# Optimization experiments

Measured on AMD Instinct MI355X. Metric: run time of the kernel, lower is better.

## Reference

```python
import jax, jax.numpy as jnp
import numpy as np

N = 100000      # number of nodes
D = 64          # node_dim
H = 128         # hidden
E = 1600000     # number of undirected edges (each yields 2 directed messages)


def setup_inputs() -> dict:
    key = jax.random.key(0)
    k_nodes, k_edges, k_w1, k_w2 = jax.random.split(key, 4)
    nodes = jax.random.normal(k_nodes, (N, D), dtype=jnp.float32)
    edges = jax.random.randint(k_edges, (E, 2), 0, N, dtype=jnp.int32)
    # msg = Linear(2D, H) -> ReLU -> Linear(H, D); Kaiming-ish init
    W1 = jax.random.normal(k_w1, (2 * D, H), dtype=jnp.float32) * (1.0 / np.sqrt(2 * D))
    b1 = jnp.zeros((H,), dtype=jnp.float32)
    W2 = jax.random.normal(k_w2, (H, D), dtype=jnp.float32) * (1.0 / np.sqrt(H))
    b2 = jnp.zeros((D,), dtype=jnp.float32)
    return {"nodes": nodes, "edges": edges, "W1": W1, "b1": b1, "W2": W2, "b2": b2}


def reference(nodes, edges, W1, b1, W2, b2):
    # nodes: [N, D]; edges: [E, 2] int32
    i = edges[:, 0]
    j = edges[:, 1]
    h_i = nodes[i]            # [E, D] gather
    h_j = nodes[j]            # [E, D] gather

    def mlp(x):               # [E, 2D] -> [E, D]
        return jax.nn.relu(x @ W1 + b1) @ W2 + b2

    m_ij = mlp(jnp.concatenate([h_i, h_j], axis=-1))  # message to node i
    m_ji = mlp(jnp.concatenate([h_j, h_i], axis=-1))  # message to node j

    # out = nodes.clone(); out[i] += m_ij; out[j] += m_ji  (all from ORIGINAL nodes)
    out = nodes \
        + jax.ops.segment_sum(m_ij, i, num_segments=N) \
        + jax.ops.segment_sum(m_ji, j, num_segments=N)
    return out
```

## Files before the change

kernel.cpp:

```cpp
#include <hip/hip_runtime.h>

#define DFEAT 64
#define NEDGES 1600000

typedef __bf16 bf16x8 __attribute__((ext_vector_type(8)));
typedef float f32x4 __attribute__((ext_vector_type(4)));

__device__ __forceinline__ __bf16 f2bf(float f) {
  unsigned u = __builtin_bit_cast(unsigned, f);
  u += 0x7FFFu + ((u >> 16) & 1u);
  unsigned short s = (unsigned short)(u >> 16);
  return __builtin_bit_cast(__bf16, s);
}

__global__ void init_out(const float* __restrict__ nodes, float* __restrict__ out) {
  int i = blockIdx.x * blockDim.x + threadIdx.x;
  ((float4*)out)[i] = ((const float4*)nodes)[i];
}

__launch_bounds__(256, 2)
__global__ void edge_mlp(const float* __restrict__ nodes,
                         const int* __restrict__ edges,
                         const float* __restrict__ W1,
                         const float* __restrict__ b1,
                         const float* __restrict__ W2,
                         const float* __restrict__ b2,
                         float* __restrict__ out) {
  __shared__ __bf16 w1t[128 * 128];
  __shared__ __bf16 w2t[64 * 128];
  __shared__ __bf16 hid[4][16 * 128];

  const int tid = threadIdx.x;

  for (int it = 0; it < 16; ++it) {
    int q = it * 256 + tid;
    int k = q >> 5;
    int nc = (q & 31) << 2;
    float4 v = ((const float4*)W1)[q];
    float vv[4] = {v.x, v.y, v.z, v.w};
#pragma unroll
    for (int c = 0; c < 4; ++c) {
      int n = nc + c;
      int blk = (k >> 3) ^ (n & 15);
      w1t[n * 128 + blk * 8 + (k & 7)] = f2bf(vv[c]);
    }
  }
  for (int it = 0; it < 8; ++it) {
    int q = it * 256 + tid;
    int k = q >> 4;
    int nc = (q & 15) << 2;
    float4 v = ((const float4*)W2)[q];
    float vv[4] = {v.x, v.y, v.z, v.w};
#pragma unroll
    for (int c = 0; c < 4; ++c) {
      int n = nc + c;
      int blk = (k >> 3) ^ (n & 15);
      w2t[n * 128 + blk * 8 + (k & 7)] = f2bf(vv[c]);
    }
  }
  __syncthreads();

  const int lane = tid & 63;
  const int wave = tid >> 6;
  const int col = lane & 15;
  const int quad = lane >> 4;
  __bf16* myhid = hid[wave];

  float b1v[8], b2v[4];
#pragma unroll
  for (int nt = 0; nt < 8; ++nt) b1v[nt] = b1[nt * 16 + col];
#pragma unroll
  for (int nt = 0; nt < 4; ++nt) b2v[nt] = b2[nt * 16 + col];

  for (int t = 0; t < 8; ++t) {
    const int e0 = blockIdx.x * 512 + wave * 128 + t * 16;
    const int e = e0 + col;
    const int ie = edges[2 * e];
    const int je = edges[2 * e + 1];

    bf16x8 af[4];
#pragma unroll
    for (int kt = 0; kt < 4; ++kt) {
      int k = kt * 32 + quad * 8;
      const float* src = (k < 64) ? (nodes + (long)ie * 64 + k)
                                  : (nodes + (long)je * 64 + (k - 64));
      float4 v0 = ((const float4*)src)[0];
      float4 v1 = ((const float4*)src)[1];
      bf16x8 a;
      a[0] = f2bf(v0.x); a[1] = f2bf(v0.y); a[2] = f2bf(v0.z); a[3] = f2bf(v0.w);
      a[4] = f2bf(v1.x); a[5] = f2bf(v1.y); a[6] = f2bf(v1.z); a[7] = f2bf(v1.w);
      af[kt] = a;
    }

#pragma unroll
    for (int dir = 0; dir < 2; ++dir) {
      f32x4 acc[8];
#pragma unroll
      for (int nt = 0; nt < 8; ++nt) acc[nt] = (f32x4)0.0f;
#pragma unroll
      for (int kt = 0; kt < 4; ++kt) {
        int kblk = kt * 4 + quad;
        if (dir) kblk ^= 8;
#pragma unroll
        for (int nt = 0; nt < 8; ++nt) {
          int n = nt * 16 + col;
          const bf16x8 bf = *(const bf16x8*)&w1t[n * 128 + ((kblk ^ (n & 15)) << 3)];
          acc[nt] = __builtin_amdgcn_mfma_f32_16x16x32_bf16(af[kt], bf, acc[nt], 0, 0, 0);
        }
      }
#pragma unroll
      for (int nt = 0; nt < 8; ++nt) {
        int unit = nt * 16 + col;
#pragma unroll
        for (int r = 0; r < 4; ++r) {
          int m = quad * 4 + r;
          float h = acc[nt][r] + b1v[nt];
          h = h > 0.0f ? h : 0.0f;
          myhid[m * 128 + (((unit >> 3) ^ m) << 3) + (unit & 7)] = f2bf(h);
        }
      }

      f32x4 acc2[4];
#pragma unroll
      for (int nt = 0; nt < 4; ++nt) acc2[nt] = (f32x4)0.0f;
#pragma unroll
      for (int kt = 0; kt < 4; ++kt) {
        int kblk = kt * 4 + quad;
        const bf16x8 ah = *(const bf16x8*)&myhid[col * 128 + ((kblk ^ col) << 3)];
#pragma unroll
        for (int nt = 0; nt < 4; ++nt) {
          int n = nt * 16 + col;
          const bf16x8 bf = *(const bf16x8*)&w2t[n * 128 + ((kblk ^ (n & 15)) << 3)];
          acc2[nt] = __builtin_amdgcn_mfma_f32_16x16x32_bf16(ah, bf, acc2[nt], 0, 0, 0);
        }
      }

#pragma unroll
      for (int r = 0; r < 4; ++r) {
        int em = quad * 4 + r;
        int node = __shfl(dir == 0 ? ie : je, em, 64);
        float* dst = out + (long)node * 64;
#pragma unroll
        for (int nt = 0; nt < 4; ++nt) {
          atomicAdd(dst + nt * 16 + col, acc2[nt][r] + b2v[nt]);
        }
      }
    }
  }
}

extern "C" void kernel_launch(void* const* d_in, const int* in_sizes, int n_in,
                              void* d_out, int out_size, void* d_ws, size_t ws_size,
                              hipStream_t stream) {
  const float* nodes = (const float*)d_in[0];
  const int*   edges = (const int*)d_in[1];
  const float* W1    = (const float*)d_in[2];
  const float* b1    = (const float*)d_in[3];
  const float* W2    = (const float*)d_in[4];
  const float* b2    = (const float*)d_in[5];
  float* out = (float*)d_out;

  init_out<<<6250, 256, 0, stream>>>(nodes, out);
  edge_mlp<<<3125, 256, 0, stream>>>(nodes, edges, W1, b1, W2, b2, out);
}
```

Measured before the change: 773.6 us.

## Compute both edge directions together with transposed MFMA and 512-thread blocks

Swaps the first-layer MFMA operands so the weights become the A operand and the gathered features the B operand, with bias preloaded into the accumulators. Both message directions are computed in one pass, so each W1 and W2 fragment loaded from LDS feeds two MFMAs, and hidden activations are written as packed bf16x4 stores. Blocks grow to 512 threads with eight waves sharing one copy of the weights in LDS, which cuts per-block weight staging. Edge indices are loaded as int2. The cost is higher register pressure from keeping two sets of accumulators live, and the launch bounds now ask for 4 blocks of 512 threads per CU.

Result: slower. 2.231 ms (+188.4%).

```diff
diff --git a/kernel.cpp b/kernel.cpp
--- a/kernel.cpp
+++ b/kernel.cpp
@@ -1,9 +1,7 @@
 #include <hip/hip_runtime.h>
 
-#define DFEAT 64
-#define NEDGES 1600000
-
 typedef __bf16 bf16x8 __attribute__((ext_vector_type(8)));
+typedef __bf16 bf16x4 __attribute__((ext_vector_type(4)));
 typedef float f32x4 __attribute__((ext_vector_type(4)));
 
 __device__ __forceinline__ __bf16 f2bf(float f) {
@@ -18,7 +16,7 @@
   ((float4*)out)[i] = ((const float4*)nodes)[i];
 }
 
-__launch_bounds__(256, 2)
+__launch_bounds__(512, 4)
 __global__ void edge_mlp(const float* __restrict__ nodes,
                          const int* __restrict__ edges,
                          const float* __restrict__ W1,
@@ -26,36 +24,36 @@
                          const float* __restrict__ W2,
                          const float* __restrict__ b2,
                          float* __restrict__ out) {
-  __shared__ __bf16 w1t[128 * 128];
+  __shared__ __bf16 w1a[128 * 128];
   __shared__ __bf16 w2t[64 * 128];
-  __shared__ __bf16 hid[4][16 * 128];
+  __shared__ __bf16 hid[8][16 * 128];
 
   const int tid = threadIdx.x;
 
-  for (int it = 0; it < 16; ++it) {
-    int q = it * 256 + tid;
+#pragma unroll
+  for (int it = 0; it < 8; ++it) {
+    int q = it * 512 + tid;
     int k = q >> 5;
-    int nc = (q & 31) << 2;
+    int u0 = (q & 31) << 2;
     float4 v = ((const float4*)W1)[q];
     float vv[4] = {v.x, v.y, v.z, v.w};
 #pragma unroll
     for (int c = 0; c < 4; ++c) {
-      int n = nc + c;
-      int blk = (k >> 3) ^ (n & 15);
-      w1t[n * 128 + blk * 8 + (k & 7)] = f2bf(vv[c]);
+      int u = u0 + c;
+      w1a[u * 128 + (((k >> 3) ^ (u & 15)) << 3) + (k & 7)] = f2bf(vv[c]);
     }
   }
-  for (int it = 0; it < 8; ++it) {
-    int q = it * 256 + tid;
+#pragma unroll
+  for (int it = 0; it < 4; ++it) {
+    int q = it * 512 + tid;
     int k = q >> 4;
-    int nc = (q & 15) << 2;
+    int n0 = (q & 15) << 2;
     float4 v = ((const float4*)W2)[q];
     float vv[4] = {v.x, v.y, v.z, v.w};
 #pragma unroll
     for (int c = 0; c < 4; ++c) {
-      int n = nc + c;
-      int blk = (k >> 3) ^ (n & 15);
-      w2t[n * 128 + blk * 8 + (k & 7)] = f2bf(vv[c]);
+      int n = n0 + c;
+      w2t[n * 128 + (((k >> 3) ^ (n & 15)) << 3) + (k & 7)] = f2bf(vv[c]);
     }
   }
   __syncthreads();
@@ -65,85 +63,104 @@
   const int col = lane & 15;
   const int quad = lane >> 4;
   __bf16* myhid = hid[wave];
+  const float4* b1q = (const float4*)b1;
 
-  float b1v[8], b2v[4];
-#pragma unroll
-  for (int nt = 0; nt < 8; ++nt) b1v[nt] = b1[nt * 16 + col];
+  float b2v[4];
 #pragma unroll
   for (int nt = 0; nt < 4; ++nt) b2v[nt] = b2[nt * 16 + col];
 
-  for (int t = 0; t < 8; ++t) {
-    const int e0 = blockIdx.x * 512 + wave * 128 + t * 16;
-    const int e = e0 + col;
-    const int ie = edges[2 * e];
-    const int je = edges[2 * e + 1];
+  for (int t = 0; t < 4; ++t) {
+    const int e0 = blockIdx.x * 512 + wave * 64 + t * 16;
+    const int2 ep = ((const int2*)edges)[e0 + col];
+    const int ie = ep.x, je = ep.y;
 
-    bf16x8 af[4];
+    bf16x8 bx[4];
 #pragma unroll
     for (int kt = 0; kt < 4; ++kt) {
       int k = kt * 32 + quad * 8;
-      const float* src = (k < 64) ? (nodes + (long)ie * 64 + k)
-                                  : (nodes + (long)je * 64 + (k - 64));
+      const float* src = (k < 64) ? (nodes + (size_t)ie * 64 + k)
+                                  : (nodes + (size_t)je * 64 + (k - 64));
       float4 v0 = ((const float4*)src)[0];
       float4 v1 = ((const float4*)src)[1];
       bf16x8 a;
       a[0] = f2bf(v0.x); a[1] = f2bf(v0.y); a[2] = f2bf(v0.z); a[3] = f2bf(v0.w);
       a[4] = f2bf(v1.x); a[5] = f2bf(v1.y); a[6] = f2bf(v1.z); a[7] = f2bf(v1.w);
-      af[kt] = a;
+      bx[kt] = a;
+    }
+
+    f32x4 acc0[8], acc1[8];
+#pragma unroll
+    for (int ut = 0; ut < 8; ++ut) {
+      float4 bi = b1q[ut * 4 + quad];
+      f32x4 b; b[0] = bi.x; b[1] = bi.y; b[2] = bi.z; b[3] = bi.w;
+      acc0[ut] = b; acc1[ut] = b;
+    }
+#pragma unroll
+    for (int kt = 0; kt < 4; ++kt) {
+      const int kb = kt * 4 + quad;
+#pragma unroll
+      for (int ut = 0; ut < 8; ++ut) {
+        const bf16x8 a = *(const bf16x8*)&w1a[(ut * 16 + col) * 128 + ((kb ^ col) << 3)];
+        acc0[ut] = __builtin_amdgcn_mfma_f32_16x16x32_bf16(a, bx[kt], acc0[ut], 0, 0, 0);
+        acc1[ut] = __builtin_amdgcn_mfma_f32_16x16x32_bf16(a, bx[kt ^ 2], acc1[ut], 0, 0, 0);
+      }
+    }
+
+    bf16x8 ah0[4], ah1[4];
+#pragma unroll
+    for (int ut = 0; ut < 8; ++ut) {
+      bf16x4 h;
+#pragma unroll
+      for (int r = 0; r < 4; ++r) {
+        float x = acc0[ut][r];
+        h[r] = f2bf(x > 0.0f ? x : 0.0f);
+      }
+      int blk = ut * 2 + (quad >> 1);
+      *(bf16x4*)&myhid[col * 128 + ((blk ^ col) << 3) + ((quad & 1) << 2)] = h;
+    }
+#pragma unroll
+    for (int kt = 0; kt < 4; ++kt)
+      ah0[kt] = *(const bf16x8*)&myhid[col * 128 + (((kt * 4 + quad) ^ col) << 3)];
+#pragma unroll
+    for (int ut = 0; ut < 8; ++ut) {
+      bf16x4 h;
+#pragma unroll
+      for (int r = 0; r < 4; ++r) {
+        float x = acc1[ut][r];
+        h[r] = f2bf(x > 0.0f ? x : 0.0f);
+      }
+      int blk = ut * 2 + (quad >> 1);
+      *(bf16x4*)&myhid[col * 128 + ((blk ^ col) << 3) + ((quad & 1) << 2)] = h;
+    }
+#pragma unroll
+    for (int kt = 0; kt < 4; ++kt)
+      ah1[kt] = *(const bf16x8*)&myhid[col * 128 + (((kt * 4 + quad) ^ col) << 3)];
+
+    f32x4 m0[4], m1[4];
+#pragma unroll
+    for (int nt = 0; nt < 4; ++nt) { m0[nt] = (f32x4)0.0f; m1[nt] = (f32x4)0.0f; }
+#pragma unroll
+    for (int kt = 0; kt < 4; ++kt) {
+      const int kb = kt * 4 + quad;
+#pragma unroll
+      for (int nt = 0; nt < 4; ++nt) {
+        const bf16x8 wf = *(const bf16x8*)&w2t[(nt * 16 + col) * 128 + ((kb ^ col) << 3)];
+        m0[nt] = __builtin_amdgcn_mfma_f32_16x16x32_bf16(ah0[kt], wf, m0[nt], 0, 0, 0);
+        m1[nt] = __builtin_amdgcn_mfma_f32_16x16x32_bf16(ah1[kt], wf, m1[nt], 0, 0, 0);
+      }
     }
 
 #pragma unroll
-    for (int dir = 0; dir < 2; ++dir) {
-      f32x4 acc[8];
+    for (int r = 0; r < 4; ++r) {
+      int row = quad * 4 + r;
+      int ni = __shfl(ie, row, 64);
+      int nj = __shfl(je, row, 64);
+      float* di = out + (size_t)ni * 64;
+      float* dj = out + (size_t)nj * 64;
 #pragma unroll
-      for (int nt = 0; nt < 8; ++nt) acc[nt] = (f32x4)0.0f;
-#pragma unroll
-      for (int kt = 0; kt < 4; ++kt) {
-        int kblk = kt * 4 + quad;
-        if (dir) kblk ^= 8;
-#pragma unroll
-        for (int nt = 0; nt < 8; ++nt) {
-          int n = nt * 16 + col;
-          const bf16x8 bf = *(const bf16x8*)&w1t[n * 128 + ((kblk ^ (n & 15)) << 3)];
-          acc[nt] = __builtin_amdgcn_mfma_f32_16x16x32_bf16(af[kt], bf, acc[nt], 0, 0, 0);
-        }
-      }
-#pragma unroll
-      for (int nt = 0; nt < 8; ++nt) {
-        int unit = nt * 16 + col;
-#pragma unroll
-        for (int r = 0; r < 4; ++r) {
-          int m = quad * 4 + r;
-          float h = acc[nt][r] + b1v[nt];
-          h = h > 0.0f ? h : 0.0f;
-          myhid[m * 128 + (((unit >> 3) ^ m) << 3) + (unit & 7)] = f2bf(h);
-        }
-      }
-
-      f32x4 acc2[4];
-#pragma unroll
-      for (int nt = 0; nt < 4; ++nt) acc2[nt] = (f32x4)0.0f;
-#pragma unroll
-      for (int kt = 0; kt < 4; ++kt) {
-        int kblk = kt * 4 + quad;
-        const bf16x8 ah = *(const bf16x8*)&myhid[col * 128 + ((kblk ^ col) << 3)];
-#pragma unroll
-        for (int nt = 0; nt < 4; ++nt) {
-          int n = nt * 16 + col;
-          const bf16x8 bf = *(const bf16x8*)&w2t[n * 128 + ((kblk ^ (n & 15)) << 3)];
-          acc2[nt] = __builtin_amdgcn_mfma_f32_16x16x32_bf16(ah, bf, acc2[nt], 0, 0, 0);
-        }
-      }
-
-#pragma unroll
-      for (int r = 0; r < 4; ++r) {
-        int em = quad * 4 + r;
-        int node = __shfl(dir == 0 ? ie : je, em, 64);
-        float* dst = out + (long)node * 64;
-#pragma unroll
-        for (int nt = 0; nt < 4; ++nt) {
-          atomicAdd(dst + nt * 16 + col, acc2[nt][r] + b2v[nt]);
-        }
+      for (int nt = 0; nt < 4; ++nt) {
+        atomicAdd(di + nt * 16 + col, m0[nt][r] + b2v[nt]);
+        atomicAdd(dj + nt * 16 + col, m1[nt][r] + b2v[nt]);
       }
     }
   }
@@ -161,5 +178,5 @@
   float* out = (float*)d_out;
 
   init_out<<<6250, 256, 0, stream>>>(nodes, out);
-  edge_mlp<<<3125, 256, 0, stream>>>(nodes, edges, W1, b1, W2, b2, out);
+  edge_mlp<<<3125, 512, 0, stream>>>(nodes, edges, W1, b1, W2, b2, out);
 }
```
